# Kernel optimization log

Measured on AMD Instinct MI355X. Metric: run time of the kernel, lower is better.

The kernel has to match this reference:

```python
import jax, jax.numpy as jnp
import numpy as np

ROW = 48   # num_row_points
COL = 48   # num_column_points
K = 21     # kernel_size


def _grid_sample_translate(ker, tx, ty):
    """Bilinear grid_sample (zeros padding, align_corners=True) for a pure
    per-image translation grid. ker: [N, h, w]; tx, ty: [N] normalized shifts.
    Matches F.affine_grid(identity + translation) + F.grid_sample."""
    N, h, w = ker.shape
    dt = ker.dtype
    # source pixel coords: px = x_out + tx*(w-1)/2 (align_corners=True)
    px = jnp.arange(w, dtype=dt)[None, :] + tx[:, None] * (w - 1) / 2  # [N, w]
    py = jnp.arange(h, dtype=dt)[None, :] + ty[:, None] * (h - 1) / 2  # [N, h]

    x0 = jnp.floor(px); fx = px - x0
    def gat_w(i):
        m = ((i >= 0) & (i <= w - 1)).astype(dt)
        ic = jnp.clip(i, 0, w - 1).astype(jnp.int32)
        v = jnp.take_along_axis(ker, jnp.broadcast_to(ic[:, None, :], ker.shape), axis=2)
        return v * m[:, None, :]
    gx = gat_w(x0) * (1 - fx)[:, None, :] + gat_w(x0 + 1) * fx[:, None, :]

    y0 = jnp.floor(py); fy = py - y0
    def gat_h(i):
        m = ((i >= 0) & (i <= h - 1)).astype(dt)
        ic = jnp.clip(i, 0, h - 1).astype(jnp.int32)
        v = jnp.take_along_axis(gx, jnp.broadcast_to(ic[:, :, None], gx.shape), axis=1)
        return v * m[:, :, None]
    return gat_h(y0) * (1 - fy)[:, :, None] + gat_h(y0 + 1) * fy[:, :, None]


def setup_inputs() -> dict:
    key = jax.random.key(0)
    k1, k2, k3 = jax.random.split(key, 3)
    N = ROW * COL
    inp = jax.random.normal(k1, (4, 64, 192, 192), dtype=jnp.float32)
    # torch.rand init; floor at 0.05 to avoid a degenerate zero sigma draw
    sigma_x = jax.random.uniform(k2, (N,), dtype=jnp.float32, minval=0.05, maxval=1.0)
    sigma_y = jax.random.uniform(k3, (N,), dtype=jnp.float32, minval=0.05, maxval=1.0)
    opacity = jnp.ones((N, 1), dtype=jnp.float32)
    return {"inp": inp, "sigma_x": sigma_x, "sigma_y": sigma_y, "opacity": opacity}


def reference(inp, sigma_x, sigma_y, opacity):
    B, C, H, W = inp.shape
    nbr, nbc = H // ROW, W // COL
    L = nbr * nbc
    N = ROW * COL

    # Unfold into non-overlapping ROWxCOL patches -> [B*L, C, ROW, COL]
    patches = (inp.reshape(B, C, nbr, ROW, nbc, COL)
                  .transpose(0, 2, 4, 1, 3, 5)
                  .reshape(B * L, C, ROW, COL))
    colors = patches.reshape(B * L, C, N).transpose(0, 2, 1)  # [BL, N, C]

    # meshgrid point coords: index k = i*COL + j, x=j (col), y=i (row)
    ii, jj = jnp.meshgrid(jnp.arange(ROW), jnp.arange(COL), indexing="ij")
    i = ii.reshape(-1).astype(inp.dtype)
    j = jj.reshape(-1).astype(inp.dtype)
    # coords_norm = (0.5 - [x/ROW, y/COL]) * 2  (note: x divided by height, as in source)
    tx = 1.0 - 2.0 * j / ROW
    ty = 1.0 - 2.0 * i / COL

    # per-point axis-aligned Gaussian kernel on [-5, 5]^2
    ax = jnp.linspace(-5.0, 5.0, K).astype(inp.dtype)
    xx2 = (ax ** 2)[None, :, None]  # x varies along first kernel dim
    yy2 = (ax ** 2)[None, None, :]
    sx2 = (sigma_x ** 2)[:, None, None]
    sy2 = (sigma_y ** 2)[:, None, None]
    z = -0.5 * (xx2 / sx2 + yy2 / sy2)                      # [N, K, K]
    kernel = jnp.exp(z) / (2.0 * jnp.pi * jnp.sqrt(sx2 * sy2))
    kernel = kernel / kernel.max(axis=(1, 2), keepdims=True)

    pad_h, pad_w = ROW - K, COL - K
    kp = jnp.pad(kernel, ((0, 0),
                          (pad_h // 2, pad_h // 2 + pad_h % 2),
                          (pad_w // 2, pad_w // 2 + pad_w % 2)))
    kt = _grid_sample_translate(kp, tx, ty)                  # [N, ROW, COL]

    weighted = colors * opacity[None, :, :]                  # [BL, N, C]
    out = jnp.einsum("bpc,phw->bchw", weighted, kt)          # splat-accumulate
    out = jnp.clip(out, 0.0, 1.0)

    # Fold back to [B, C, H, W]
    out = (out.reshape(B, nbr, nbc, C, ROW, COL)
              .transpose(0, 3, 1, 4, 2, 5)
              .reshape(B, C, H, W))
    return out
```

## Files before the change

kernel.cpp:

```cpp
#include <hip/hip_runtime.h>


#define NPTS 2304
#define KD   2304
#define HH   192

typedef _Float16 f16;
typedef _Float16 f16x8 __attribute__((ext_vector_type(8)));
typedef float f32x4 __attribute__((ext_vector_type(4)));

__device__ __forceinline__ void gload16(const f16* g, f16* l) {
    __builtin_amdgcn_global_load_lds((const __attribute__((address_space(1))) void*)g,
                                     (__attribute__((address_space(3))) void*)l,
                                     16, 0, 0);
}

__device__ __forceinline__ float gtap(float t, float inv2s) {
    float ax = 0.5f * t - 11.5f;
    float g = expf(-ax * ax * inv2s);
    return (t >= 12.5f && t <= 33.5f) ? g : 0.0f;
}

__global__ void build_kt(const float* __restrict__ sx, const float* __restrict__ sy,
                         const float* __restrict__ op, f16* __restrict__ Kt) {
    int idx = blockIdx.x * 256 + threadIdx.x;
    int hw = idx / 288;
    int p0 = (idx - hw * 288) * 8;
    int y = hw / 48, x = hw - y * 48;
    int i = p0 / 48, j0 = p0 - i * 48;

    float py = (float)y + 23.5f - (47.0f / 48.0f) * (float)i;
    float y0 = floorf(py), fy = py - y0;

    f16x8 r;
    #pragma unroll
    for (int u = 0; u < 8; ++u) {
        int p = p0 + u;
        float sxv = sx[p], syv = sy[p], opv = op[p];
        float invx = 0.5f / (sxv * sxv);
        float invy = 0.5f / (syv * syv);
        float ky = opv * (gtap(y0, invx) * (1.0f - fy) + gtap(y0 + 1.0f, invx) * fy);
        float px = (float)x + 23.5f - (47.0f / 48.0f) * (float)(j0 + u);
        float x0 = floorf(px), fx = px - x0;
        float kx = gtap(x0, invy) * (1.0f - fx) + gtap(x0 + 1.0f, invy) * fx;
        r[u] = (f16)(ky * kx);
    }
    *(f16x8*)(Kt + (size_t)hw * NPTS + p0) = r;
}

__global__ void pack_A(const float* __restrict__ inp, f16* __restrict__ A) {
    int idx = blockIdx.x * 256 + threadIdx.x;
    int m = idx / 288;
    int p0 = (idx - m * 288) * 8;
    int i = p0 / 48, j = p0 - i * 48;
    int bl = m >> 6, c = m & 63;
    int b = bl >> 4, pr = (bl >> 2) & 3, pc = bl & 3;
    const float* src = inp + ((size_t)(b * 64 + c) * HH + pr * 48 + i) * HH + pc * 48 + j;
    float4 a0 = *(const float4*)src;
    float4 a1 = *(const float4*)(src + 4);
    f16x8 r;
    r[0] = (f16)a0.x; r[1] = (f16)a0.y; r[2] = (f16)a0.z; r[3] = (f16)a0.w;
    r[4] = (f16)a1.x; r[5] = (f16)a1.y; r[6] = (f16)a1.z; r[7] = (f16)a1.w;
    *(f16x8*)(A + (size_t)m * KD + p0) = r;
}

__global__ __launch_bounds__(256) void gemm_splat(const f16* __restrict__ A,
                                                  const f16* __restrict__ Bt,
                                                  float* __restrict__ out) {
    __shared__ __attribute__((aligned(16))) f16 As[2 * 4096];
    __shared__ __attribute__((aligned(16))) f16 Bs[2 * 4096];

    int tid  = threadIdx.x;
    int lane = tid & 63;
    int w    = tid >> 6;
    int wr   = w >> 1, wc = w & 1;
    int bx   = blockIdx.x;
    int wg   = (bx & 7) * 72 + (bx >> 3);
    int m0   = (wg / 18) * 128;
    int n0   = (wg % 18) * 128;

    int y_min = n0 / 48;
    int y_max = (n0 + 127) / 48;
    int i_lo = max(0,  (int)floorf((y_min - 10.5f) * (48.0f / 47.0f)));
    int i_hi = min(47, (int)ceilf ((y_max + 11.5f) * (48.0f / 47.0f)));
    int k_lo = (i_lo * 48) & ~31;
    int k_hi = min(KD, ((i_hi + 1) * 48 + 31) & ~31);
    int nt   = (k_hi - k_lo) >> 5;

    int srow = lane >> 2;
    int sk   = (((lane & 3) ^ ((lane >> 3) & 3)) << 3);
    const f16* Abase = A  + (size_t)(m0 + w * 32 + srow) * KD + sk + k_lo;
    const f16* Bbase = Bt + (size_t)(n0 + w * 32 + srow) * KD + sk + k_lo;

    int lrow = lane & 15;
    int koe  = (((lane >> 4) ^ ((lane >> 1) & 3)) << 3);

    f32x4 acc[4][4] = {};

    #define STAGE(buf, koff)                                                          \
        do {                                                                          \
            gload16(Abase + (koff),            &As[(buf) * 4096 + w * 1024]);         \
            gload16(Abase + 16 * KD + (koff),  &As[(buf) * 4096 + w * 1024 + 512]);   \
            gload16(Bbase + (koff),            &Bs[(buf) * 4096 + w * 1024]);         \
            gload16(Bbase + 16 * KD + (koff),  &Bs[(buf) * 4096 + w * 1024 + 512]);   \
        } while (0)

    STAGE(0, 0);
    __syncthreads();

    for (int t = 0; t < nt; ++t) {
        int cur = t & 1;
        if (t + 1 < nt) STAGE(cur ^ 1, (t + 1) << 5);

        f16x8 af[4], bf[4];
        #pragma unroll
        for (int mi = 0; mi < 4; ++mi)
            af[mi] = *(const f16x8*)&As[cur * 4096 + (wr * 64 + mi * 16 + lrow) * 32 + koe];
        #pragma unroll
        for (int ni = 0; ni < 4; ++ni)
            bf[ni] = *(const f16x8*)&Bs[cur * 4096 + (wc * 64 + ni * 16 + lrow) * 32 + koe];

        #pragma unroll
        for (int mi = 0; mi < 4; ++mi)
            #pragma unroll
            for (int ni = 0; ni < 4; ++ni)
                acc[mi][ni] = __builtin_amdgcn_mfma_f32_16x16x32_f16(af[mi], bf[ni], acc[mi][ni], 0, 0, 0);

        __syncthreads();
    }
    #undef STAGE

    #pragma unroll
    for (int mi = 0; mi < 4; ++mi) {
        #pragma unroll
        for (int r = 0; r < 4; ++r) {
            int m  = m0 + wr * 64 + mi * 16 + (lane >> 4) * 4 + r;
            int bl = m >> 6, c = m & 63;
            int b  = bl >> 4, pr = (bl >> 2) & 3, pc = bl & 3;
            float* orow = out + ((size_t)(b * 64 + c) * HH + pr * 48) * HH + pc * 48;
            #pragma unroll
            for (int ni = 0; ni < 4; ++ni) {
                int n = n0 + wc * 64 + ni * 16 + (lane & 15);
                int y = n / 48, x = n - y * 48;
                float v = acc[mi][ni][r];
                v = fminf(fmaxf(v, 0.0f), 1.0f);
                orow[y * HH + x] = v;
            }
        }
    }
}

extern "C" void kernel_launch(void* const* d_in, const int* in_sizes, int n_in,
                              void* d_out, int out_size, void* d_ws, size_t ws_size,
                              hipStream_t stream) {
    const float* inp = (const float*)d_in[0];
    const float* sx  = (const float*)d_in[1];
    const float* sy  = (const float*)d_in[2];
    const float* op  = (const float*)d_in[3];
    float* out = (float*)d_out;

    char* ws = (char*)d_ws;
    f16* Kt = (f16*)ws;
    f16* Ap = (f16*)(ws + 10616832);

    build_kt  <<<dim3(2592), dim3(256), 0, stream>>>(sx, sy, op, Kt);
    pack_A    <<<dim3(4608), dim3(256), 0, stream>>>(inp, Ap);
    gemm_splat<<<dim3(576),  dim3(256), 0, stream>>>(Ap, Kt, out);
}
```

Before: 138.4 us.

## Triple-buffer GEMM LDS pipeline and merge prep kernels into one launch

The GEMM's LDS staging moves from two buffers to three, so loads run two tiles ahead. Explicit vmcnt waits and raw s_barrier replace the per-iteration __syncthreads, and s_setprio raises priority around the MFMA block. The two preprocessing kernels (kernel build and input pack) are fused into one launch that branches on block index, removing one launch and its inter-kernel gap. The cost is more LDS per block, which may lower occupancy, plus hand-counted waitcnt logic that must stay correct.

Measured after the change: 137.6 us. Within noise of the previous version (-0.5%).

```diff
diff --git a/kernel.cpp b/kernel.cpp
--- a/kernel.cpp
+++ b/kernel.cpp
@@ -21,54 +21,55 @@
     return (t >= 12.5f && t <= 33.5f) ? g : 0.0f;
 }
 
-__global__ void build_kt(const float* __restrict__ sx, const float* __restrict__ sy,
-                         const float* __restrict__ op, f16* __restrict__ Kt) {
-    int idx = blockIdx.x * 256 + threadIdx.x;
-    int hw = idx / 288;
-    int p0 = (idx - hw * 288) * 8;
-    int y = hw / 48, x = hw - y * 48;
-    int i = p0 / 48, j0 = p0 - i * 48;
-
-    float py = (float)y + 23.5f - (47.0f / 48.0f) * (float)i;
-    float y0 = floorf(py), fy = py - y0;
-
-    f16x8 r;
-    #pragma unroll
-    for (int u = 0; u < 8; ++u) {
-        int p = p0 + u;
-        float sxv = sx[p], syv = sy[p], opv = op[p];
-        float invx = 0.5f / (sxv * sxv);
-        float invy = 0.5f / (syv * syv);
-        float ky = opv * (gtap(y0, invx) * (1.0f - fy) + gtap(y0 + 1.0f, invx) * fy);
-        float px = (float)x + 23.5f - (47.0f / 48.0f) * (float)(j0 + u);
-        float x0 = floorf(px), fx = px - x0;
-        float kx = gtap(x0, invy) * (1.0f - fx) + gtap(x0 + 1.0f, invy) * fx;
-        r[u] = (f16)(ky * kx);
+__global__ void prep(const float* __restrict__ inp,
+                     const float* __restrict__ sx, const float* __restrict__ sy,
+                     const float* __restrict__ op,
+                     f16* __restrict__ Kt, f16* __restrict__ Ap) {
+    int bid = blockIdx.x;
+    if (bid < 2592) {
+        int idx = bid * 256 + threadIdx.x;
+        int hw = idx / 288;
+        int p0 = (idx - hw * 288) * 8;
+        int y = hw / 48, x = hw - y * 48;
+        int i = p0 / 48, j0 = p0 - i * 48;
+        float py = (float)y + 23.5f - (47.0f / 48.0f) * (float)i;
+        float y0 = floorf(py), fy = py - y0;
+        f16x8 r;
+        #pragma unroll
+        for (int u = 0; u < 8; ++u) {
+            int p = p0 + u;
+            float sxv = sx[p], syv = sy[p], opv = op[p];
+            float invx = 0.5f / (sxv * sxv);
+            float invy = 0.5f / (syv * syv);
+            float ky = opv * (gtap(y0, invx) * (1.0f - fy) + gtap(y0 + 1.0f, invx) * fy);
+            float px = (float)x + 23.5f - (47.0f / 48.0f) * (float)(j0 + u);
+            float x0 = floorf(px), fx = px - x0;
+            float kx = gtap(x0, invy) * (1.0f - fx) + gtap(x0 + 1.0f, invy) * fx;
+            r[u] = (f16)(ky * kx);
+        }
+        *(f16x8*)(Kt + (size_t)hw * NPTS + p0) = r;
+    } else {
+        int idx = (bid - 2592) * 256 + threadIdx.x;
+        int m = idx / 288;
+        int p0 = (idx - m * 288) * 8;
+        int i = p0 / 48, j = p0 - i * 48;
+        int bl = m >> 6, c = m & 63;
+        int b = bl >> 4, pr = (bl >> 2) & 3, pc = bl & 3;
+        const float* src = inp + ((size_t)(b * 64 + c) * HH + pr * 48 + i) * HH + pc * 48 + j;
+        float4 a0 = *(const float4*)src;
+        float4 a1 = *(const float4*)(src + 4);
+        f16x8 r;
+        r[0] = (f16)a0.x; r[1] = (f16)a0.y; r[2] = (f16)a0.z; r[3] = (f16)a0.w;
+        r[4] = (f16)a1.x; r[5] = (f16)a1.y; r[6] = (f16)a1.z; r[7] = (f16)a1.w;
+        *(f16x8*)(Ap + (size_t)m * KD + p0) = r;
     }
-    *(f16x8*)(Kt + (size_t)hw * NPTS + p0) = r;
-}
-
-__global__ void pack_A(const float* __restrict__ inp, f16* __restrict__ A) {
-    int idx = blockIdx.x * 256 + threadIdx.x;
-    int m = idx / 288;
-    int p0 = (idx - m * 288) * 8;
-    int i = p0 / 48, j = p0 - i * 48;
-    int bl = m >> 6, c = m & 63;
-    int b = bl >> 4, pr = (bl >> 2) & 3, pc = bl & 3;
-    const float* src = inp + ((size_t)(b * 64 + c) * HH + pr * 48 + i) * HH + pc * 48 + j;
-    float4 a0 = *(const float4*)src;
-    float4 a1 = *(const float4*)(src + 4);
-    f16x8 r;
-    r[0] = (f16)a0.x; r[1] = (f16)a0.y; r[2] = (f16)a0.z; r[3] = (f16)a0.w;
-    r[4] = (f16)a1.x; r[5] = (f16)a1.y; r[6] = (f16)a1.z; r[7] = (f16)a1.w;
-    *(f16x8*)(A + (size_t)m * KD + p0) = r;
 }
 
 __global__ __launch_bounds__(256) void gemm_splat(const f16* __restrict__ A,
                                                   const f16* __restrict__ Bt,
                                                   float* __restrict__ out) {
-    __shared__ __attribute__((aligned(16))) f16 As[2 * 4096];
-    __shared__ __attribute__((aligned(16))) f16 Bs[2 * 4096];
+    __shared__ __attribute__((aligned(16))) f16 As[3 * 4096];
+    __shared__ __attribute__((aligned(16))) f16 Bs[3 * 4096];
 
     int tid  = threadIdx.x;
     int lane = tid & 63;
@@ -97,36 +98,55 @@
 
     f32x4 acc[4][4] = {};
 
-    #define STAGE(buf, koff)                                                          \
-        do {                                                                          \
-            gload16(Abase + (koff),            &As[(buf) * 4096 + w * 1024]);         \
-            gload16(Abase + 16 * KD + (koff),  &As[(buf) * 4096 + w * 1024 + 512]);   \
-            gload16(Bbase + (koff),            &Bs[(buf) * 4096 + w * 1024]);         \
-            gload16(Bbase + 16 * KD + (koff),  &Bs[(buf) * 4096 + w * 1024 + 512]);   \
+    #define STAGE(slot, koff)                                                   \
+        do {                                                                    \
+            f16* as_ = &As[(slot) * 4096 + w * 1024];                           \
+            f16* bs_ = &Bs[(slot) * 4096 + w * 1024];                           \
+            gload16(Abase + (koff),           as_);                             \
+            gload16(Abase + 16 * KD + (koff), as_ + 512);                       \
+            gload16(Bbase + (koff),           bs_);                             \
+            gload16(Bbase + 16 * KD + (koff), bs_ + 512);                       \
         } while (0)
 
     STAGE(0, 0);
-    __syncthreads();
+    STAGE(1, 32);
+    asm volatile("s_waitcnt vmcnt(4)" ::: "memory");
+    __builtin_amdgcn_s_barrier();
+    __builtin_amdgcn_sched_barrier(0);
 
+    int rs = 0, ps = 2;
     for (int t = 0; t < nt; ++t) {
-        int cur = t & 1;
-        if (t + 1 < nt) STAGE(cur ^ 1, (t + 1) << 5);
+        if (t + 2 < nt) STAGE(ps, (t + 2) << 5);
 
+        const f16* as_ = &As[rs * 4096];
+        const f16* bs_ = &Bs[rs * 4096];
         f16x8 af[4], bf[4];
         #pragma unroll
         for (int mi = 0; mi < 4; ++mi)
-            af[mi] = *(const f16x8*)&As[cur * 4096 + (wr * 64 + mi * 16 + lrow) * 32 + koe];
+            af[mi] = *(const f16x8*)&as_[(wr * 64 + mi * 16 + lrow) * 32 + koe];
         #pragma unroll
         for (int ni = 0; ni < 4; ++ni)
-            bf[ni] = *(const f16x8*)&Bs[cur * 4096 + (wc * 64 + ni * 16 + lrow) * 32 + koe];
+            bf[ni] = *(const f16x8*)&bs_[(wc * 64 + ni * 16 + lrow) * 32 + koe];
 
+        __builtin_amdgcn_s_setprio(1);
         #pragma unroll
         for (int mi = 0; mi < 4; ++mi)
             #pragma unroll
             for (int ni = 0; ni < 4; ++ni)
                 acc[mi][ni] = __builtin_amdgcn_mfma_f32_16x16x32_f16(af[mi], bf[ni], acc[mi][ni], 0, 0, 0);
+        __builtin_amdgcn_s_setprio(0);
 
-        __syncthreads();
+        if (t + 2 < nt) {
+            asm volatile("s_waitcnt vmcnt(4)" ::: "memory");
+        } else if (t + 1 < nt) {
+            asm volatile("s_waitcnt vmcnt(0)" ::: "memory");
+        }
+        if (t + 1 < nt) {
+            __builtin_amdgcn_s_barrier();
+            __builtin_amdgcn_sched_barrier(0);
+        }
+        ps = rs;
+        rs = (rs == 2) ? 0 : rs + 1;
     }
     #undef STAGE
 
@@ -163,7 +183,6 @@
     f16* Kt = (f16*)ws;
     f16* Ap = (f16*)(ws + 10616832);
 
-    build_kt  <<<dim3(2592), dim3(256), 0, stream>>>(sx, sy, op, Kt);
-    pack_A    <<<dim3(4608), dim3(256), 0, stream>>>(inp, Ap);
+    prep      <<<dim3(7200), dim3(256), 0, stream>>>(inp, sx, sy, op, Kt, Ap);
     gemm_splat<<<dim3(576),  dim3(256), 0, stream>>>(Ap, Kt, out);
 }
```
